# Kernel optimization log

Hardware: AMD Instinct MI355X
Metric: run time of the kernel (lower is better)

The kernel has to match this reference:

```python
import jax, jax.numpy as jnp
import numpy as np
import math

N = 3072      # number of graph nodes
D = 256       # in_dim == out_dim
H = 8         # heads
EPS = 1e-5    # LayerNorm eps (torch default)


def _glorot(key, shape):
    fan = shape[-2] + shape[-1]
    std = math.sqrt(6.0 / fan)
    return jax.random.uniform(key, shape, jnp.float32, -std, std)


def layer_norm(x, g, b):
    mu = jnp.mean(x, axis=-1, keepdims=True)
    var = jnp.mean(jnp.square(x - mu), axis=-1, keepdims=True)
    return (x - mu) * jax.lax.rsqrt(var + EPS) * g + b


def setup_inputs() -> dict:
    key = jax.random.key(0)
    ks = jax.random.split(key, 12)
    input_x = jax.random.normal(ks[0], (N, D), jnp.float32)
    # degrees: positive floats in [1, 50)
    deg = 1.0 + 49.0 * jax.random.uniform(ks[1], (N,), jnp.float32)
    WQ = _glorot(ks[2], (H, D, D))
    WK = _glorot(ks[3], (H, D, D))
    WV = _glorot(ks[4], (H, D, D))
    # linears stored as [in, out] (math-equivalent to torch's [out,in] transposed)
    lin_attn_w = _glorot(ks[5], (H * D, D)); lin_attn_b = jnp.zeros((D,), jnp.float32)
    lin_w = _glorot(ks[6], (2 * D, D));       lin_b = jnp.zeros((D,), jnp.float32)
    fnn1_w = _glorot(ks[7], (D, D));          fnn1_b = jnp.zeros((D,), jnp.float32)
    fnn2_w = _glorot(ks[8], (D, D));          fnn2_b = jnp.zeros((D,), jnp.float32)
    ln1_g = jnp.ones((D,), jnp.float32); ln1_b = jnp.zeros((D,), jnp.float32)
    ln2_g = jnp.ones((D,), jnp.float32); ln2_b = jnp.zeros((D,), jnp.float32)
    return dict(input_x=input_x, deg=deg, WQ=WQ, WK=WK, WV=WV,
                lin_attn_w=lin_attn_w, lin_attn_b=lin_attn_b,
                lin_w=lin_w, lin_b=lin_b,
                ln1_g=ln1_g, ln1_b=ln1_b,
                fnn1_w=fnn1_w, fnn1_b=fnn1_b,
                fnn2_w=fnn2_w, fnn2_b=fnn2_b,
                ln2_g=ln2_g, ln2_b=ln2_b)


def reference(input_x, deg, WQ, WK, WV, lin_attn_w, lin_attn_b,
              lin_w, lin_b, ln1_g, ln1_b, fnn1_w, fnn1_b,
              fnn2_w, fnn2_b, ln2_g, ln2_b):
    n = input_x.shape[0]
    # --- multi-head attention over all nodes ---
    Q = jnp.einsum('nd,hde->hne', input_x, WQ)   # [H,N,D]
    K = jnp.einsum('nd,hde->hne', input_x, WK)
    V = jnp.einsum('nd,hde->hne', input_x, WV)
    scores = jnp.einsum('hne,hme->hnm', Q, K)    # [H,N,N]
    # diagonal self-mask: QKT[i] += diag_embed(diag(QKT[i]) - 1e20)
    idx = jnp.arange(n)
    diag_vals = scores[:, idx, idx]
    scores = scores.at[:, idx, idx].add(diag_vals - 1e20)
    attn = jax.nn.softmax(scores / math.sqrt(D), axis=-1)
    attn_x = jnp.einsum('hnm,hme->hne', attn, V)           # [H,N,D]
    attn_cat = jnp.transpose(attn_x, (1, 0, 2)).reshape(n, H * D)
    attn_out = attn_cat @ lin_attn_w + lin_attn_b          # [N,D]
    # --- degree-norm concat + residual + LN ---
    x1 = jnp.concatenate([input_x, attn_out / jnp.sqrt(deg)[:, None]], axis=-1)
    x1 = x1 @ lin_w + lin_b
    x1 = layer_norm(input_x + x1, ln1_g, ln1_b)
    # --- FFN block (dropout inactive at eval) ---
    x2 = jax.nn.relu(x1 @ fnn1_w + fnn1_b)
    x2 = x2 @ fnn2_w + fnn2_b
    return layer_norm(x1 + x2, ln2_g, ln2_b)
```

## Files before the change

### kernel.cpp

```cpp
#include <hip/hip_runtime.h>
#include <hip/hip_bf16.h>
#include <stdint.h>

typedef __bf16 bf16x8_t __attribute__((ext_vector_type(8)));
typedef short  s16x8_t  __attribute__((ext_vector_type(8)));
typedef unsigned short u16x4_t __attribute__((ext_vector_type(4)));
typedef unsigned short u16x8_t __attribute__((ext_vector_type(8)));
typedef float  f32x4_t __attribute__((ext_vector_type(4)));

#define NTOK 3072
#define NHEAD 8
#define NSPLIT 4

__device__ __forceinline__ unsigned short f2bf(float f) {
  union { float f; uint32_t u; } v; v.f = f;
  uint32_t r = v.u + 0x7fffu + ((v.u >> 16) & 1u);
  return (unsigned short)(r >> 16);
}
__device__ __forceinline__ float bf2f(unsigned short s) {
  union { uint32_t u; float f; } v; v.u = ((uint32_t)s) << 16;
  return v.f;
}

__device__ __forceinline__ void gload_lds16(const void* g, void* lds) {
  __builtin_amdgcn_global_load_lds(
      (const __attribute__((address_space(1))) uint32_t*)g,
      (__attribute__((address_space(3))) uint32_t*)lds, 16, 0, 0);
}

template <int CTRL>
__device__ __forceinline__ float dpp_mv(float x) {
  union { float f; int i; } u; u.f = x;
  u.i = __builtin_amdgcn_update_dpp(0, u.i, CTRL, 0xf, 0xf, true);
  return u.f;
}
__device__ __forceinline__ float red_max16(float x) {
  x = fmaxf(x, dpp_mv<0xB1>(x));
  x = fmaxf(x, dpp_mv<0x4E>(x));
  x = fmaxf(x, dpp_mv<0x141>(x));
  x = fmaxf(x, dpp_mv<0x140>(x));
  return x;
}
__device__ __forceinline__ float red_sum16(float x) {
  x += dpp_mv<0xB1>(x);
  x += dpp_mv<0x4E>(x);
  x += dpp_mv<0x141>(x);
  x += dpp_mv<0x140>(x);
  return x;
}

__global__ void prep_all(const float* __restrict__ WQ, const float* __restrict__ WK,
                         const float* __restrict__ WV, const float* __restrict__ law,
                         const float* __restrict__ lw, const float* __restrict__ f1w,
                         const float* __restrict__ f2w, const float* __restrict__ x,
                         unsigned short* __restrict__ qkvwT, unsigned short* __restrict__ lawT,
                         unsigned short* __restrict__ lwT, unsigned short* __restrict__ f1T,
                         unsigned short* __restrict__ f2T, unsigned short* __restrict__ xa) {
  __shared__ float tile[64][65];
  const int id = blockIdx.x;
  const int t = threadIdx.x;
  if (id >= 576) {
    int n0 = (id - 576) * 64;
    int col = (t & 63) * 4;
#pragma unroll
    for (int i = 0; i < 16; ++i) {
      int n = n0 + i * 4 + (t >> 6);
      f32x4_t v = *(const f32x4_t*)(x + (size_t)n * 256 + col);
      u16x4_t o;
#pragma unroll
      for (int j = 0; j < 4; ++j) o[j] = f2bf(v[j]);
      *(u16x4_t*)(xa + (size_t)n * 512 + col) = o;
    }
    return;
  }
  const float* src; unsigned short* dst; int sld, dld, d0, e0;
  if (id < 384) {
    int z = id >> 4, tl = id & 15;
    int op = z >> 3, hh = z & 7;
    src = ((op == 0) ? WQ : (op == 1) ? WK : WV) + (size_t)hh * 65536;
    dst = qkvwT + (size_t)z * 65536;
    sld = 256; dld = 256; d0 = (tl >> 2) * 64; e0 = (tl & 3) * 64;
  } else if (id < 512) {
    int tl = id - 384;
    src = law; dst = lawT; sld = 256; dld = 2048;
    d0 = (tl >> 2) * 64; e0 = (tl & 3) * 64;
  } else if (id < 544) {
    int tl = id - 512;
    src = lw; dst = lwT; sld = 256; dld = 512;
    d0 = (tl >> 2) * 64; e0 = (tl & 3) * 64;
  } else if (id < 560) {
    int tl = id - 544;
    src = f1w; dst = f1T; sld = 256; dld = 256;
    d0 = (tl >> 2) * 64; e0 = (tl & 3) * 64;
  } else {
    int tl = id - 560;
    src = f2w; dst = f2T; sld = 256; dld = 256;
    d0 = (tl >> 2) * 64; e0 = (tl & 3) * 64;
  }
  int tr = t >> 4, tc4 = (t & 15) * 4;
#pragma unroll
  for (int i = 0; i < 4; ++i) {
    int d = i * 16 + tr;
    f32x4_t v = *(const f32x4_t*)(src + (size_t)(d0 + d) * sld + e0 + tc4);
    tile[d][tc4] = v[0]; tile[d][tc4 + 1] = v[1]; tile[d][tc4 + 2] = v[2]; tile[d][tc4 + 3] = v[3];
  }
  __syncthreads();
#pragma unroll
  for (int i = 0; i < 4; ++i) {
    int e = i * 16 + tr;
    u16x4_t o;
#pragma unroll
    for (int j = 0; j < 4; ++j) o[j] = f2bf(tile[tc4 + j][e]);
    *(u16x4_t*)(dst + (size_t)(e0 + e) * dld + d0 + tc4) = o;
  }
}

template <int BM, int BN>
__global__ __launch_bounds__(256, 2) void gemm_kernel(
    const unsigned short* __restrict__ A, int lda,
    const unsigned short* __restrict__ B, int ldb,
    void* __restrict__ Cout, int ldc, int Klen,
    const float* __restrict__ bias,
    const float* __restrict__ resid, int ldr,
    const float* __restrict__ deg, int flags,
    float* __restrict__ part, long pstride) {
  constexpr int WM = BM / 2, WN = BN / 2, FM = WM / 16, FN = WN / 16;
  __shared__ unsigned short As[BM * 32];
  __shared__ unsigned short Bs[BN * 32];
  const int t = threadIdx.x;
  const int w = t >> 6, l = t & 63;
  const int l15 = l & 15, lhi = l >> 4;
  const int row0 = blockIdx.y * BM, col0 = blockIdx.x * BN;
  const int wr = (w >> 1) * WM, wc = (w & 1) * WN;

  f32x4_t acc[FM][FN];
#pragma unroll
  for (int m = 0; m < FM; ++m)
#pragma unroll
    for (int n = 0; n < FN; ++n) acc[m][n] = (f32x4_t){0.f, 0.f, 0.f, 0.f};

  const int srow = l >> 2;
  const int spc  = (l & 3) * 16;
  const int kofs0 = blockIdx.z * Klen;
  const int nkt = Klen >> 5;
  for (int kt = 0; kt < nkt; ++kt) {
    const int koff = kofs0 + kt * 32;
    __syncthreads();
#pragma unroll
    for (int c = w; c < BM / 16; c += 4) {
      int ar = c * 16 + srow;
      int lcb = spc ^ (((ar >> 1) & 3) << 4);
      gload_lds16(A + (size_t)(row0 + ar) * lda + koff + (lcb >> 1), &As[c * 512]);
    }
#pragma unroll
    for (int c = w; c < BN / 16; c += 4) {
      int br = c * 16 + srow;
      int lcb = spc ^ (((br >> 1) & 3) << 4);
      gload_lds16(B + (size_t)(col0 + br) * ldb + koff + (lcb >> 1), &Bs[c * 512]);
    }
    __syncthreads();
    bf16x8_t af[FM], bfr[FN];
#pragma unroll
    for (int m = 0; m < FM; ++m) {
      int ar = wr + m * 16 + l15;
      af[m] = *(const bf16x8_t*)(&As[(ar * 64 + ((lhi * 16) ^ (((ar >> 1) & 3) << 4))) >> 1]);
    }
#pragma unroll
    for (int n = 0; n < FN; ++n) {
      int br = wc + n * 16 + l15;
      bfr[n] = *(const bf16x8_t*)(&Bs[(br * 64 + ((lhi * 16) ^ (((br >> 1) & 3) << 4))) >> 1]);
    }
#pragma unroll
    for (int m = 0; m < FM; ++m)
#pragma unroll
      for (int n = 0; n < FN; ++n)
        acc[m][n] = __builtin_amdgcn_mfma_f32_16x16x32_bf16(af[m], bfr[n], acc[m][n], 0, 0, 0);
  }

  const bool relu = flags & 1, obf = flags & 2, dsc = flags & 4, ppart = flags & 8;
#pragma unroll
  for (int m = 0; m < FM; ++m) {
#pragma unroll
    for (int r = 0; r < 4; ++r) {
      int grow = row0 + wr + m * 16 + lhi * 4 + r;
      float sc = dsc ? rsqrtf(deg[grow]) : 1.0f;
#pragma unroll
      for (int n = 0; n < FN; ++n) {
        int gcol = col0 + wc + n * 16 + l15;
        float v = acc[m][n][r];
        if (ppart) {
          part[(size_t)blockIdx.z * pstride + (size_t)grow * ldc + gcol] = v;
          continue;
        }
        if (bias) v += bias[gcol];
        v *= sc;
        if (resid) v += resid[(size_t)grow * ldr + gcol];
        if (relu) v = fmaxf(v, 0.f);
        if (obf)
          ((unsigned short*)Cout)[(size_t)grow * ldc + gcol] = f2bf(v);
        else
          ((float*)Cout)[(size_t)grow * ldc + gcol] = v;
      }
    }
  }
}

__global__ void attn_reduce(const float* __restrict__ part, const float* __restrict__ lab,
                            const float* __restrict__ deg, unsigned short* __restrict__ xa) {
  int n = blockIdx.x, d = threadIdx.x;
  float s = 0.f;
#pragma unroll
  for (int z = 0; z < 4; ++z) s += part[((size_t)z * NTOK + n) * 256 + d];
  xa[(size_t)n * 512 + 256 + d] = f2bf((s + lab[d]) * rsqrtf(deg[n]));
}

#define VSW64(e) (((((e) & 7) ^ (((e) >> 3) & 7))) << 4)
#define PSW(r)   (((r) & 7) << 4)
__global__ __launch_bounds__(256, 2) void flash_kernel(
    const unsigned short* __restrict__ qkv, unsigned short* __restrict__ pO,
    float* __restrict__ ml) {
  __shared__ unsigned short Ks[64 * 256];
  __shared__ unsigned short Vt[256 * 64];
  __shared__ unsigned short Ps[4][16 * 64];
  const int bid = blockIdx.x;
  const int hs = bid % (NHEAD * NSPLIT);
  const int qb = bid / (NHEAD * NSPLIT);
  const int h = hs / NSPLIT;
  const int split = hs % NSPLIT;
  const int q0 = qb * 64;
  const int t = threadIdx.x, w = t >> 6, l = t & 63;
  const int l15 = l & 15, lhi = l >> 4;

  const int vn0 = (t & 7) * 8;
  const int ve0 = (t >> 3) * 8;

  bf16x8_t qf[8];
  {
    const unsigned short* Qb = qkv + (size_t)(q0 + w * 16 + l15) * 6144 + h * 256 + lhi * 8;
#pragma unroll
    for (int kk = 0; kk < 8; ++kk) qf[kk] = *(const bf16x8_t*)(Qb + kk * 32);
  }
  f32x4_t o[16];
#pragma unroll
  for (int et = 0; et < 16; ++et) o[et] = (f32x4_t){0.f, 0.f, 0.f, 0.f};
  float m_run[4] = {-1e30f, -1e30f, -1e30f, -1e30f};
  float l_run[4] = {0.f, 0.f, 0.f, 0.f};

  for (int it = 0; it < 12; ++it) {
    const int kv0 = (split * 12 + it) * 64;
    __syncthreads();
    {
      int rh = l >> 5;
      int pc = (l & 31) * 16;
#pragma unroll
      for (int i = 0; i < 8; ++i) {
        int c = w * 8 + i;
        int kr = c * 2 + rh;
        int lcb = pc ^ ((kr & 7) << 4);
        gload_lds16(qkv + (size_t)(kv0 + kr) * 6144 + 2048 + h * 256 + (lcb >> 1), &Ks[c * 512]);
      }
    }
    {
      s16x8_t rv[8];
      const unsigned short* Vg = qkv + (size_t)(kv0 + vn0) * 6144 + 4096 + h * 256 + ve0;
#pragma unroll
      for (int rr = 0; rr < 8; ++rr) rv[rr] = *(const s16x8_t*)(Vg + rr * 6144);
#pragma unroll
      for (int j = 0; j < 8; ++j) {
        int e = ve0 + j;
        u16x8_t pk;
#pragma unroll
        for (int rr = 0; rr < 8; ++rr) pk[rr] = (unsigned short)rv[rr][j];
        int pb = e * 128 + ((vn0 * 2) ^ VSW64(e));
        *(u16x8_t*)(&Vt[pb >> 1]) = pk;
      }
    }
    __syncthreads();

    f32x4_t s[4];
#pragma unroll
    for (int ni = 0; ni < 4; ++ni) s[ni] = (f32x4_t){0.f, 0.f, 0.f, 0.f};
    __builtin_amdgcn_s_setprio(1);
#pragma unroll
    for (int kk = 0; kk < 8; ++kk) {
#pragma unroll
      for (int ni = 0; ni < 4; ++ni) {
        int br = ni * 16 + l15;
        bf16x8_t kb = *(const bf16x8_t*)(&Ks[(br * 512 + ((kk * 64 + lhi * 16) ^ ((br & 7) << 4))) >> 1]);
        s[ni] = __builtin_amdgcn_mfma_f32_16x16x32_bf16(qf[kk], kb, s[ni], 0, 0, 0);
      }
    }
    __builtin_amdgcn_s_setprio(0);

    float p[4][4];
    float alpha[4];
#pragma unroll
    for (int r = 0; r < 4; ++r) {
      int grow = q0 + w * 16 + lhi * 4 + r;
      float sv[4];
      float mx0 = -1e30f, mx1 = -1e30f;
#pragma unroll
      for (int ni = 0; ni < 4; ++ni) {
        float x = s[ni][r] * 0.0625f;
        if (kv0 + ni * 16 + l15 == grow) x = -1e30f;
        sv[ni] = x;
        if (ni & 1) mx1 = fmaxf(mx1, x); else mx0 = fmaxf(mx0, x);
      }
      float mx = red_max16(fmaxf(mx0, mx1));
      float mn = fmaxf(m_run[r], mx);
      alpha[r] = __expf(m_run[r] - mn);
      m_run[r] = mn;
      float ls = 0.f;
#pragma unroll
      for (int ni = 0; ni < 4; ++ni) {
        float pv = __expf(sv[ni] - mn);
        p[ni][r] = pv;
        ls += pv;
      }
      ls = red_sum16(ls);
      l_run[r] = l_run[r] * alpha[r] + ls;
    }
#pragma unroll
    for (int et = 0; et < 16; ++et)
#pragma unroll
      for (int r = 0; r < 4; ++r) o[et][r] *= alpha[r];

    unsigned short* Pw = &Ps[w][0];
#pragma unroll
    for (int ni = 0; ni < 4; ++ni)
#pragma unroll
      for (int r = 0; r < 4; ++r) {
        int prow = lhi * 4 + r;
        int pb = prow * 128 + (((ni * 16 + l15) * 2) ^ PSW(prow));
        Pw[pb >> 1] = f2bf(p[ni][r]);
      }
    bf16x8_t pa0 = *(const bf16x8_t*)(&Pw[(l15 * 128 + ((lhi * 16) ^ PSW(l15))) >> 1]);
    bf16x8_t pa1 = *(const bf16x8_t*)(&Pw[(l15 * 128 + ((64 + lhi * 16) ^ PSW(l15))) >> 1]);
    __builtin_amdgcn_s_setprio(1);
#pragma unroll
    for (int et = 0; et < 16; ++et) {
      int er = et * 16 + l15;
      bf16x8_t vb0 = *(const bf16x8_t*)(&Vt[(er * 128 + ((lhi * 16) ^ VSW64(er))) >> 1]);
      bf16x8_t vb1 = *(const bf16x8_t*)(&Vt[(er * 128 + ((64 + lhi * 16) ^ VSW64(er))) >> 1]);
      o[et] = __builtin_amdgcn_mfma_f32_16x16x32_bf16(pa0, vb0, o[et], 0, 0, 0);
      o[et] = __builtin_amdgcn_mfma_f32_16x16x32_bf16(pa1, vb1, o[et], 0, 0, 0);
    }
    __builtin_amdgcn_s_setprio(0);
  }

  const size_t sh = (size_t)(split * NHEAD + h);
#pragma unroll
  for (int et = 0; et < 16; ++et)
#pragma unroll
    for (int r = 0; r < 4; ++r) {
      int grow = q0 + w * 16 + lhi * 4 + r;
      pO[(sh * NTOK + grow) * 256 + et * 16 + l15] = f2bf(o[et][r]);
    }
  if (l15 == 0) {
#pragma unroll
    for (int r = 0; r < 4; ++r) {
      int grow = q0 + w * 16 + lhi * 4 + r;
      ml[(sh * NTOK + grow) * 2] = m_run[r];
      ml[(sh * NTOK + grow) * 2 + 1] = l_run[r];
    }
  }
}

__global__ void flash_combine(const unsigned short* __restrict__ pO,
                              const float* __restrict__ ml,
                              unsigned short* __restrict__ acat) {
  int n = blockIdx.x, t = threadIdx.x;
  int h = t >> 5, e0 = (t & 31) * 8;
  float ms[NSPLIT], ls[NSPLIT];
  float M = -1e30f;
#pragma unroll
  for (int s = 0; s < NSPLIT; ++s) {
    size_t b = ((size_t)(s * NHEAD + h) * NTOK + n) * 2;
    ms[s] = ml[b]; ls[s] = ml[b + 1];
    M = fmaxf(M, ms[s]);
  }
  float den = 0.f;
  float num[8];
#pragma unroll
  for (int j = 0; j < 8; ++j) num[j] = 0.f;
#pragma unroll
  for (int s = 0; s < NSPLIT; ++s) {
    float ws = __expf(ms[s] - M);
    den += ws * ls[s];
    s16x8_t ov = *(const s16x8_t*)(pO + ((size_t)(s * NHEAD + h) * NTOK + n) * 256 + e0);
#pragma unroll
    for (int j = 0; j < 8; ++j) num[j] += ws * bf2f((unsigned short)ov[j]);
  }
  float rden = 1.0f / den;
  s16x8_t out;
#pragma unroll
  for (int j = 0; j < 8; ++j) out[j] = (short)f2bf(num[j] * rden);
  *(s16x8_t*)(acat + (size_t)n * 2048 + h * 256 + e0) = out;
}

__global__ __launch_bounds__(256, 2) void tail_fused(
    const unsigned short* __restrict__ xa, const unsigned short* __restrict__ lwT,
    const unsigned short* __restrict__ f1T, const unsigned short* __restrict__ f2T,
    const float* __restrict__ x, const float* __restrict__ lb,
    const float* __restrict__ ln1g, const float* __restrict__ ln1b,
    const float* __restrict__ f1b, const float* __restrict__ f2b,
    const float* __restrict__ ln2g, const float* __restrict__ ln2b,
    float* __restrict__ out) {
  __shared__ unsigned short As[16 * 32];
  __shared__ unsigned short Bs[256 * 32];
  __shared__ unsigned short Xs[16 * 256];
  __shared__ float red[16][4][2];
  const int t = threadIdx.x, w = t >> 6, l = t & 63;
  const int l15 = l & 15, lhi = l >> 4;
  const int row0 = blockIdx.x * 16;
  const int wc = w * 64;
  const int srow = l >> 2, spc = (l & 3) * 16;

  f32x4_t acc[4];
#pragma unroll
  for (int n = 0; n < 4; ++n) acc[n] = (f32x4_t){0.f, 0.f, 0.f, 0.f};
  for (int kt = 0; kt < 16; ++kt) {
    __syncthreads();
    if (w == 0) {
      int ar = srow;
      int lcb = spc ^ (((ar >> 1) & 3) << 4);
      gload_lds16(xa + (size_t)(row0 + ar) * 512 + kt * 32 + (lcb >> 1), &As[0]);
    }
#pragma unroll
    for (int c = w; c < 16; c += 4) {
      int br = c * 16 + srow;
      int lcb = spc ^ (((br >> 1) & 3) << 4);
      gload_lds16(lwT + (size_t)br * 512 + kt * 32 + (lcb >> 1), &Bs[c * 512]);
    }
    __syncthreads();
    bf16x8_t af = *(const bf16x8_t*)(&As[(l15 * 64 + ((lhi * 16) ^ (((l15 >> 1) & 3) << 4))) >> 1]);
#pragma unroll
    for (int n = 0; n < 4; ++n) {
      int br = wc + n * 16 + l15;
      bf16x8_t bfr = *(const bf16x8_t*)(&Bs[(br * 64 + ((lhi * 16) ^ (((br >> 1) & 3) << 4))) >> 1]);
      acc[n] = __builtin_amdgcn_mfma_f32_16x16x32_bf16(af, bfr, acc[n], 0, 0, 0);
    }
  }
  float x1v[4][4];
#pragma unroll
  for (int r = 0; r < 4; ++r) {
    int grow = row0 + lhi * 4 + r;
#pragma unroll
    for (int n = 0; n < 4; ++n) {
      int col = wc + n * 16 + l15;
      x1v[n][r] = acc[n][r] + lb[col] + x[(size_t)grow * 256 + col];
    }
  }
#pragma unroll
  for (int r = 0; r < 4; ++r) {
    float s = x1v[0][r] + x1v[1][r] + x1v[2][r] + x1v[3][r];
    float q = x1v[0][r] * x1v[0][r] + x1v[1][r] * x1v[1][r] +
              x1v[2][r] * x1v[2][r] + x1v[3][r] * x1v[3][r];
    s = red_sum16(s); q = red_sum16(q);
    if (l15 == 0) { red[lhi * 4 + r][w][0] = s; red[lhi * 4 + r][w][1] = q; }
  }
  __syncthreads();
#pragma unroll
  for (int r = 0; r < 4; ++r) {
    int row = lhi * 4 + r;
    float s = red[row][0][0] + red[row][1][0] + red[row][2][0] + red[row][3][0];
    float q = red[row][0][1] + red[row][1][1] + red[row][2][1] + red[row][3][1];
    float mu = s * (1.0f / 256.0f);
    float var = q * (1.0f / 256.0f) - mu * mu;
    float rstd = rsqrtf(var + 1e-5f);
#pragma unroll
    for (int n = 0; n < 4; ++n) {
      int col = wc + n * 16 + l15;
      float xv = (x1v[n][r] - mu) * rstd * ln1g[col] + ln1b[col];
      x1v[n][r] = xv;
      int pb = row * 512 + ((col * 2) ^ ((row & 7) << 4));
      Xs[pb >> 1] = f2bf(xv);
    }
  }

  f32x4_t acc2[4];
#pragma unroll
  for (int n = 0; n < 4; ++n) acc2[n] = (f32x4_t){0.f, 0.f, 0.f, 0.f};
  for (int kt = 0; kt < 8; ++kt) {
    __syncthreads();
#pragma unroll
    for (int c = w; c < 16; c += 4) {
      int br = c * 16 + srow;
      int lcb = spc ^ (((br >> 1) & 3) << 4);
      gload_lds16(f1T + (size_t)br * 256 + kt * 32 + (lcb >> 1), &Bs[c * 512]);
    }
    __syncthreads();
    bf16x8_t af = *(const bf16x8_t*)(&Xs[(l15 * 512 + (((kt * 32 + lhi * 8) * 2) ^ ((l15 & 7) << 4))) >> 1]);
#pragma unroll
    for (int n = 0; n < 4; ++n) {
      int br = wc + n * 16 + l15;
      bf16x8_t bfr = *(const bf16x8_t*)(&Bs[(br * 64 + ((lhi * 16) ^ (((br >> 1) & 3) << 4))) >> 1]);
      acc2[n] = __builtin_amdgcn_mfma_f32_16x16x32_bf16(af, bfr, acc2[n], 0, 0, 0);
    }
  }
  __syncthreads();
#pragma unroll
  for (int r = 0; r < 4; ++r) {
    int row = lhi * 4 + r;
#pragma unroll
    for (int n = 0; n < 4; ++n) {
      int col = wc + n * 16 + l15;
      float v = fmaxf(acc2[n][r] + f1b[col], 0.f);
      int pb = row * 512 + ((col * 2) ^ ((row & 7) << 4));
      Xs[pb >> 1] = f2bf(v);
    }
  }

  f32x4_t acc3[4];
#pragma unroll
  for (int n = 0; n < 4; ++n) acc3[n] = (f32x4_t){0.f, 0.f, 0.f, 0.f};
  for (int kt = 0; kt < 8; ++kt) {
    __syncthreads();
#pragma unroll
    for (int c = w; c < 16; c += 4) {
      int br = c * 16 + srow;
      int lcb = spc ^ (((br >> 1) & 3) << 4);
      gload_lds16(f2T + (size_t)br * 256 + kt * 32 + (lcb >> 1), &Bs[c * 512]);
    }
    __syncthreads();
    bf16x8_t af = *(const bf16x8_t*)(&Xs[(l15 * 512 + (((kt * 32 + lhi * 8) * 2) ^ ((l15 & 7) << 4))) >> 1]);
#pragma unroll
    for (int n = 0; n < 4; ++n) {
      int br = wc + n * 16 + l15;
      bf16x8_t bfr = *(const bf16x8_t*)(&Bs[(br * 64 + ((lhi * 16) ^ (((br >> 1) & 3) << 4))) >> 1]);
      acc3[n] = __builtin_amdgcn_mfma_f32_16x16x32_bf16(af, bfr, acc3[n], 0, 0, 0);
    }
  }
  float u2v[4][4];
#pragma unroll
  for (int r = 0; r < 4; ++r) {
#pragma unroll
    for (int n = 0; n < 4; ++n) {
      int col = wc + n * 16 + l15;
      u2v[n][r] = acc3[n][r] + f2b[col] + x1v[n][r];
    }
  }
  __syncthreads();
#pragma unroll
  for (int r = 0; r < 4; ++r) {
    float s = u2v[0][r] + u2v[1][r] + u2v[2][r] + u2v[3][r];
    float q = u2v[0][r] * u2v[0][r] + u2v[1][r] * u2v[1][r] +
              u2v[2][r] * u2v[2][r] + u2v[3][r] * u2v[3][r];
    s = red_sum16(s); q = red_sum16(q);
    if (l15 == 0) { red[lhi * 4 + r][w][0] = s; red[lhi * 4 + r][w][1] = q; }
  }
  __syncthreads();
#pragma unroll
  for (int r = 0; r < 4; ++r) {
    int row = lhi * 4 + r;
    int grow = row0 + row;
    float s = red[row][0][0] + red[row][1][0] + red[row][2][0] + red[row][3][0];
    float q = red[row][0][1] + red[row][1][1] + red[row][2][1] + red[row][3][1];
    float mu = s * (1.0f / 256.0f);
    float var = q * (1.0f / 256.0f) - mu * mu;
    float rstd = rsqrtf(var + 1e-5f);
#pragma unroll
    for (int n = 0; n < 4; ++n) {
      int col = wc + n * 16 + l15;
      out[(size_t)grow * 256 + col] = (u2v[n][r] - mu) * rstd * ln2g[col] + ln2b[col];
    }
  }
}

extern "C" void kernel_launch(void* const* d_in, const int* in_sizes, int n_in,
                              void* d_out, int out_size, void* d_ws, size_t ws_size,
                              hipStream_t stream) {
  const float* x    = (const float*)d_in[0];
  const float* deg  = (const float*)d_in[1];
  const float* WQ   = (const float*)d_in[2];
  const float* WK   = (const float*)d_in[3];
  const float* WV   = (const float*)d_in[4];
  const float* law  = (const float*)d_in[5];
  const float* lab  = (const float*)d_in[6];
  const float* lw   = (const float*)d_in[7];
  const float* lb   = (const float*)d_in[8];
  const float* ln1g = (const float*)d_in[9];
  const float* ln1b = (const float*)d_in[10];
  const float* f1w  = (const float*)d_in[11];
  const float* f1b  = (const float*)d_in[12];
  const float* f2w  = (const float*)d_in[13];
  const float* f2b  = (const float*)d_in[14];
  const float* ln2g = (const float*)d_in[15];
  const float* ln2b = (const float*)d_in[16];

  char* ws = (char*)d_ws;
  size_t off = 0;
  auto alloc = [&](size_t bytes) {
    void* p = ws + off;
    off += (bytes + 255) & ~(size_t)255;
    return p;
  };
  unsigned short* qkvwT = (unsigned short*)alloc((size_t)6144 * 256 * 2);
  unsigned short* lawT  = (unsigned short*)alloc((size_t)256 * 2048 * 2);
  unsigned short* lwT   = (unsigned short*)alloc((size_t)256 * 512 * 2);
  unsigned short* f1T   = (unsigned short*)alloc((size_t)256 * 256 * 2);
  unsigned short* f2T   = (unsigned short*)alloc((size_t)256 * 256 * 2);
  unsigned short* xa    = (unsigned short*)alloc((size_t)NTOK * 512 * 2);
  unsigned short* qkv   = (unsigned short*)alloc((size_t)NTOK * 6144 * 2);
  unsigned short* acat  = (unsigned short*)alloc((size_t)NTOK * 2048 * 2);
  unsigned short* pO    = (unsigned short*)alloc((size_t)NSPLIT * NHEAD * NTOK * 256 * 2);
  float*          mlp   = (float*)alloc((size_t)NSPLIT * NHEAD * NTOK * 2 * 4);
  float*          apart = (float*)alloc((size_t)4 * NTOK * 256 * 4);

  prep_all<<<624, 256, 0, stream>>>(WQ, WK, WV, law, lw, f1w, f2w, x,
                                    qkvwT, lawT, lwT, f1T, f2T, xa);

  gemm_kernel<128, 128><<<dim3(48, 24), 256, 0, stream>>>(
      xa, 512, qkvwT, 256, qkv, 6144, 256, nullptr, nullptr, 0, nullptr, 2, nullptr, 0);

  flash_kernel<<<NTOK / 64 * NHEAD * NSPLIT, 256, 0, stream>>>(qkv, pO, mlp);
  flash_combine<<<NTOK, 256, 0, stream>>>(pO, mlp, acat);

  gemm_kernel<64, 64><<<dim3(4, 48, 4), 256, 0, stream>>>(
      acat, 2048, lawT, 2048, nullptr, 256, 512, nullptr, nullptr, 0, nullptr, 8,
      apart, (long)NTOK * 256);
  attn_reduce<<<NTOK, 256, 0, stream>>>(apart, lab, deg, xa);

  tail_fused<<<NTOK / 16, 256, 0, stream>>>(
      xa, lwT, f1T, f2T, x, lb, ln1g, ln1b, f1b, f2b, ln2g, ln2b, (float*)d_out);
}
```

Measured before the change: 324.8 us.

## Prefetch next K/V tile during softmax and skip rescale unless max jumps

The flash attention loop now issues the next tile's async K load and V register loads right after the QK^T MFMAs. Their latency hides behind the softmax and PV work, and V is transposed into LDS only after PV, behind an extra barrier. It also adds lazy online-softmax rescaling: the output accumulators and running sum are rescaled only when some row's new max exceeds the running max by more than 8. This cuts per-tile multiply work. The cost is more registers held for the prefetched V and unnormalized exponentials up to e^8 in bf16 P.

```diff
diff --git a/kernel.cpp b/kernel.cpp
--- a/kernel.cpp
+++ b/kernel.cpp
@@ -234,6 +234,34 @@
   const int vn0 = (t & 7) * 8;
   const int ve0 = (t >> 3) * 8;
 
+  auto issueK = [&](int kv0) {
+    int rh = l >> 5;
+    int pc = (l & 31) * 16;
+#pragma unroll
+    for (int i = 0; i < 8; ++i) {
+      int c = w * 8 + i;
+      int kr = c * 2 + rh;
+      int lcb = pc ^ ((kr & 7) << 4);
+      gload_lds16(qkv + (size_t)(kv0 + kr) * 6144 + 2048 + h * 256 + (lcb >> 1), &Ks[c * 512]);
+    }
+  };
+  auto issueV = [&](int kv0, s16x8_t rv[8]) {
+    const unsigned short* Vg = qkv + (size_t)(kv0 + vn0) * 6144 + 4096 + h * 256 + ve0;
+#pragma unroll
+    for (int rr = 0; rr < 8; ++rr) rv[rr] = *(const s16x8_t*)(Vg + rr * 6144);
+  };
+  auto packV = [&](s16x8_t rv[8]) {
+#pragma unroll
+    for (int j = 0; j < 8; ++j) {
+      int e = ve0 + j;
+      u16x8_t pk;
+#pragma unroll
+      for (int rr = 0; rr < 8; ++rr) pk[rr] = (unsigned short)rv[rr][j];
+      int pb = e * 128 + ((vn0 * 2) ^ VSW64(e));
+      *(u16x8_t*)(&Vt[pb >> 1]) = pk;
+    }
+  };
+
   bf16x8_t qf[8];
   {
     const unsigned short* Qb = qkv + (size_t)(q0 + w * 16 + l15) * 6144 + h * 256 + lhi * 8;
@@ -246,36 +274,17 @@
   float m_run[4] = {-1e30f, -1e30f, -1e30f, -1e30f};
   float l_run[4] = {0.f, 0.f, 0.f, 0.f};
 
+  {
+    s16x8_t rva[8];
+    issueV((split * 12) * 64, rva);
+    issueK((split * 12) * 64);
+    packV(rva);
+  }
+  __syncthreads();
+
   for (int it = 0; it < 12; ++it) {
     const int kv0 = (split * 12 + it) * 64;
-    __syncthreads();
-    {
-      int rh = l >> 5;
-      int pc = (l & 31) * 16;
-#pragma unroll
-      for (int i = 0; i < 8; ++i) {
-        int c = w * 8 + i;
-        int kr = c * 2 + rh;
-        int lcb = pc ^ ((kr & 7) << 4);
-        gload_lds16(qkv + (size_t)(kv0 + kr) * 6144 + 2048 + h * 256 + (lcb >> 1), &Ks[c * 512]);
-      }
-    }
-    {
-      s16x8_t rv[8];
-      const unsigned short* Vg = qkv + (size_t)(kv0 + vn0) * 6144 + 4096 + h * 256 + ve0;
-#pragma unroll
-      for (int rr = 0; rr < 8; ++rr) rv[rr] = *(const s16x8_t*)(Vg + rr * 6144);
-#pragma unroll
-      for (int j = 0; j < 8; ++j) {
-        int e = ve0 + j;
-        u16x8_t pk;
-#pragma unroll
-        for (int rr = 0; rr < 8; ++rr) pk[rr] = (unsigned short)rv[rr][j];
-        int pb = e * 128 + ((vn0 * 2) ^ VSW64(e));
-        *(u16x8_t*)(&Vt[pb >> 1]) = pk;
-      }
-    }
-    __syncthreads();
+    const bool have_nxt = (it + 1 < 12);
 
     f32x4_t s[4];
 #pragma unroll
@@ -291,39 +300,60 @@
       }
     }
     __builtin_amdgcn_s_setprio(0);
-
-    float p[4][4];
-    float alpha[4];
+    __syncthreads();
+
+    s16x8_t rvb[8];
+    if (have_nxt) {
+      issueV(kv0 + 64, rvb);
+      issueK(kv0 + 64);
+    }
+
+    float svv[4][4];
+    float mxr[4];
 #pragma unroll
     for (int r = 0; r < 4; ++r) {
       int grow = q0 + w * 16 + lhi * 4 + r;
-      float sv[4];
       float mx0 = -1e30f, mx1 = -1e30f;
 #pragma unroll
       for (int ni = 0; ni < 4; ++ni) {
         float x = s[ni][r] * 0.0625f;
         if (kv0 + ni * 16 + l15 == grow) x = -1e30f;
-        sv[ni] = x;
+        svv[ni][r] = x;
         if (ni & 1) mx1 = fmaxf(mx1, x); else mx0 = fmaxf(mx0, x);
       }
-      float mx = red_max16(fmaxf(mx0, mx1));
-      float mn = fmaxf(m_run[r], mx);
-      alpha[r] = __expf(m_run[r] - mn);
-      m_run[r] = mn;
+      mxr[r] = red_max16(fmaxf(mx0, mx1));
+    }
+    float needf = mxr[0] - m_run[0];
+    needf = fmaxf(needf, mxr[1] - m_run[1]);
+    needf = fmaxf(needf, mxr[2] - m_run[2]);
+    needf = fmaxf(needf, mxr[3] - m_run[3]);
+    if (__any(needf > 8.0f)) {
+      float alpha[4];
+#pragma unroll
+      for (int r = 0; r < 4; ++r) {
+        float mn = fmaxf(m_run[r], mxr[r]);
+        alpha[r] = __expf(m_run[r] - mn);
+        m_run[r] = mn;
+        l_run[r] *= alpha[r];
+      }
+#pragma unroll
+      for (int et = 0; et < 16; ++et)
+#pragma unroll
+        for (int r = 0; r < 4; ++r) o[et][r] *= alpha[r];
+    }
+    float p[4][4];
+#pragma unroll
+    for (int r = 0; r < 4; ++r) {
       float ls = 0.f;
 #pragma unroll
       for (int ni = 0; ni < 4; ++ni) {
-        float pv = __expf(sv[ni] - mn);
+        float pv = __expf(svv[ni][r] - m_run[r]);
         p[ni][r] = pv;
         ls += pv;
       }
       ls = red_sum16(ls);
-      l_run[r] = l_run[r] * alpha[r] + ls;
-    }
-#pragma unroll
-    for (int et = 0; et < 16; ++et)
-#pragma unroll
-      for (int r = 0; r < 4; ++r) o[et][r] *= alpha[r];
+      l_run[r] += ls;
+    }
 
     unsigned short* Pw = &Ps[w][0];
 #pragma unroll
@@ -346,6 +376,11 @@
       o[et] = __builtin_amdgcn_mfma_f32_16x16x32_bf16(pa1, vb1, o[et], 0, 0, 0);
     }
     __builtin_amdgcn_s_setprio(0);
+
+    if (have_nxt) {
+      __syncthreads();
+      packV(rvb);
+    }
   }
 
   const size_t sh = (size_t)(split * NHEAD + h);
```

After: 327.7 us. About the same (+0.9%).
